# Kernel optimization log

Measured on AMD Instinct MI355X. Metric: run time of the kernel, lower is better.

## Reference

```python
import jax, jax.numpy as jnp
import numpy as np
from jax import lax

C = 16
FIRE_RATE = 0.5
STEP_SIZE = 1.0


def _fixed_kernel():
    _i = np.array([0, 1, 0], dtype=np.float32)
    I = np.outer(_i, _i)
    dx = (np.outer([1, 2, 1], [-1, 0, 1]) / 8.0).astype(np.float32)
    dy = dx.T
    lap = np.array([[0.25, 0.5, 0.25], [0.5, -3, 0.5], [0.25, 0.5, 0.25]], dtype=np.float32)
    av = np.ones((3, 3), dtype=np.float32) / 9.0
    k = np.stack([I, dx, dy, lap, av], -1)            # [3,3,5]
    k = np.tile(k, (1, 1, C))                          # [3,3,5*C], channel-major blocks of 5
    return jnp.asarray(k[:, :, None, :])               # HWIO [3,3,1,5*C]

KERNEL = _fixed_kernel()


def setup_inputs() -> dict:
    key = jax.random.key(0)
    ks = jax.random.split(key, 5)
    B, S = 4, 512
    x = jax.random.normal(ks[0], (B, S, S, C), jnp.float32)
    noise = jax.random.normal(ks[1], (B, S, S, 1), jnp.float32)
    W1 = jax.random.normal(ks[2], (5 * C, 4 * C), jnp.float32) * (1.0 / np.sqrt(5 * C))
    b1 = jnp.zeros((4 * C,), jnp.float32)
    W2 = jax.random.normal(ks[3], (4 * C, 2 * C), jnp.float32) * (1.0 / np.sqrt(4 * C))
    b2 = jnp.zeros((2 * C,), jnp.float32)
    W3 = jax.random.normal(ks[4], (2 * C, C), jnp.float32) * (1.0 / np.sqrt(2 * C))
    b3 = jnp.zeros((C,), jnp.float32)
    return {"x": x, "noise": noise, "W1": W1, "b1": b1, "W2": W2, "b2": b2, "W3": W3, "b3": b3}


def _swish(z):
    return z * jax.nn.sigmoid(z)


def reference(x, noise, W1, b1, W2, b2, W3, b3):
    # perceive: depthwise 3x3 conv with 5 fixed kernels per channel -> [B,H,W,5*C]
    y = lax.conv_general_dilated(
        x, KERNEL, window_strides=(1, 1), padding="SAME",
        dimension_numbers=("NHWC", "HWIO", "NHWC"), feature_group_count=C)
    # 3-layer 1x1 conv MLP
    h = _swish(jnp.einsum("bhwc,cd->bhwd", y, W1) + b1)
    h = _swish(jnp.einsum("bhwc,cd->bhwd", h, W2) + b2)
    dx = (jnp.einsum("bhwc,cd->bhwd", h, W3) + b3) * STEP_SIZE
    # stochastic update mask: normal noise <= fire_rate
    update_mask = (noise <= FIRE_RATE).astype(jnp.float32)  # [B,H,W,1]
    return x + dx * update_mask
```

## Files before the change

kernel.cpp:

```cpp
#include <hip/hip_runtime.h>

typedef __bf16 bf16x8 __attribute__((ext_vector_type(8)));
typedef float f32x4 __attribute__((ext_vector_type(4)));
typedef float f32x16 __attribute__((ext_vector_type(16)));
typedef short short8 __attribute__((ext_vector_type(8)));

#define S 512
#define CH 16

#define ELT(v, c) ((c)==0 ? (v).x : (c)==1 ? (v).y : (c)==2 ? (v).z : (v).w)

__device__ __forceinline__ float swishf(float z) {
    return z * __builtin_amdgcn_rcpf(1.0f + __expf(-z));
}

__global__ void prep_weights(const float* __restrict__ W1, const float* __restrict__ b1,
                             const float* __restrict__ W2, const float* __restrict__ b2,
                             const float* __restrict__ W3, const float* __restrict__ b3,
                             short* __restrict__ wsf, float* __restrict__ wsb)
{
    int idx = blockIdx.x * 256 + threadIdx.x;
    if (idx < 7680) {
        float v;
        if (idx < 5120) {
            int fi = idx >> 9, rem = idx & 511;
            int lane = rem >> 3, j = rem & 7;
            int n = fi / 5, s = fi - n * 5;
            int blk = lane >> 5, colw = lane & 31;
            int m = s * 8 + j, cc = m / 5, f = m - cc * 5;
            int row = (blk * 8 + cc) * 5 + f;
            v = W1[row * 64 + n * 32 + colw];
        } else if (idx < 7168) {
            int i2 = idx - 5120;
            int fi = i2 >> 9, rem = i2 & 511;
            int lane = rem >> 3, j = rem & 7;
            int u2 = fi >> 1, t = fi & 1;
            int k = t * 32 + (lane >> 4) * 8 + j;
            v = W2[k * 32 + u2 * 16 + (lane & 15)];
        } else {
            int i3 = idx - 7168;
            int lane = i3 >> 3, j = i3 & 7;
            int k = (lane >> 4) * 8 + j;
            v = W3[k * 16 + (lane & 15)];
        }
        __bf16 b = (__bf16)v;
        wsf[idx] = __builtin_bit_cast(short, b);
    }
    if (blockIdx.x == 0) {
        int t = threadIdx.x;
        if (t < 64) wsb[t] = b1[t];
        else if (t < 96) wsb[t] = b2[t - 64];
        else if (t < 112) wsb[t] = b3[t - 96];
    }
}

__global__ __launch_bounds__(256, 4) void nca_fused(
    const float* __restrict__ x, const float* __restrict__ noise,
    const short* __restrict__ wsf, const float* __restrict__ wsb,
    float* __restrict__ out)
{
    __shared__ short wlds[7680];
    __shared__ __bf16 h1s[4][32][72];
    __shared__ __bf16 h2s[4][16][40];

    const int tid = threadIdx.x;
    {
        const int4* src = reinterpret_cast<const int4*>(wsf);
        int4* dst = reinterpret_cast<int4*>(wlds);
        for (int i = tid; i < 960; i += 256) dst[i] = src[i];
    }
    __syncthreads();

    const int bid = blockIdx.x;
    const int st = bid & 7;
    const int rg = (bid >> 3) & 127;
    const int bb = bid >> 10;
    const int wv = tid >> 6;
    const int lane = tid & 63;
    const int col = lane & 31, hi = lane >> 5;
    const int lr = lane & 15, lg = lane >> 4;
    const int row = rg * 4 + wv;

    float b1v[2], b2v[2], b3v;
    b1v[0] = wsb[col];        b1v[1] = wsb[32 + col];
    b2v[0] = wsb[64 + lr];    b2v[1] = wsb[80 + lr];
    b3v = wsb[96 + lr];

    const bool rv0 = row > 0, rv2 = row < S - 1;
    const float* xb = x + (size_t)bb * S * S * CH;
    const short8* wf = reinterpret_cast<const short8*>(wlds);

#pragma unroll
    for (int mt = 0; mt < 2; ++mt) {
        const int px0 = st * 64 + mt * 32;
        const bool colInt = (px0 != 0) && (px0 != 480);
        const int p = col;

        short8 af[5];
#pragma unroll
        for (int qi = 0; qi < 2; ++qi) {
            const int q = hi * 2 + qi;
            float4 A[3][3];
#pragma unroll
            for (int rr = 0; rr < 3; ++rr) {
                bool rok = (rr == 0) ? rv0 : (rr == 2 ? rv2 : true);
                if (rok) {
                    const float* rp = xb + (size_t)(row - 1 + rr) * S * CH + q * 4;
                    if (colInt) {
                        const float* bp = rp + (px0 + p - 1) * CH;
                        A[rr][0] = *reinterpret_cast<const float4*>(bp);
                        A[rr][1] = *reinterpret_cast<const float4*>(bp + CH);
                        A[rr][2] = *reinterpret_cast<const float4*>(bp + 2 * CH);
                    } else {
#pragma unroll
                        for (int d = 0; d < 3; ++d) {
                            int c = px0 + p - 1 + d;
                            int cl = min(max(c, 0), S - 1);
                            float4 v = *reinterpret_cast<const float4*>(rp + cl * CH);
                            if ((unsigned)c >= (unsigned)S) v = make_float4(0.f, 0.f, 0.f, 0.f);
                            A[rr][d] = v;
                        }
                    }
                } else {
                    A[rr][0] = make_float4(0.f, 0.f, 0.f, 0.f);
                    A[rr][1] = A[rr][0]; A[rr][2] = A[rr][0];
                }
            }
#pragma unroll
            for (int cc = 0; cc < 4; ++cc) {
                float a00 = ELT(A[0][0], cc), a01 = ELT(A[0][1], cc), a02 = ELT(A[0][2], cc);
                float a10 = ELT(A[1][0], cc), a11 = ELT(A[1][1], cc), a12 = ELT(A[1][2], cc);
                float a20 = ELT(A[2][0], cc), a21 = ELT(A[2][1], cc), a22 = ELT(A[2][2], cc);
                float cw0 = a00 + 2.f * a10 + a20;
                float cw1 = a01 + 2.f * a11 + a21;
                float cw2 = a02 + 2.f * a12 + a22;
                float rw0 = a00 + 2.f * a01 + a02;
                float rw2 = a20 + 2.f * a21 + a22;
                float fI  = a11;
                float fdx = (cw2 - cw0) * 0.125f;
                float fdy = (rw2 - rw0) * 0.125f;
                float flp = 0.25f * (cw0 + 2.f * cw1 + cw2) - 4.f * a11;
                float fav = ((cw0 + cw1 + cw2) - (a10 + a11 + a12)) * (1.f / 9.f);
                const int mb = (qi * 4 + cc) * 5;
                af[(mb + 0) >> 3][(mb + 0) & 7] = __builtin_bit_cast(short, (__bf16)fI);
                af[(mb + 1) >> 3][(mb + 1) & 7] = __builtin_bit_cast(short, (__bf16)fdx);
                af[(mb + 2) >> 3][(mb + 2) & 7] = __builtin_bit_cast(short, (__bf16)fdy);
                af[(mb + 3) >> 3][(mb + 3) & 7] = __builtin_bit_cast(short, (__bf16)flp);
                af[(mb + 4) >> 3][(mb + 4) & 7] = __builtin_bit_cast(short, (__bf16)fav);
            }
        }

#pragma unroll
        for (int n = 0; n < 2; ++n) {
            f32x16 acc = {};
#pragma unroll
            for (int s = 0; s < 5; ++s) {
                bf16x8 a = __builtin_bit_cast(bf16x8, af[s]);
                bf16x8 b = __builtin_bit_cast(bf16x8, wf[(n * 5 + s) * 64 + lane]);
                acc = __builtin_amdgcn_mfma_f32_32x32x16_bf16(a, b, acc, 0, 0, 0);
            }
#pragma unroll
            for (int r = 0; r < 16; ++r) {
                int p2 = (r & 3) + 8 * (r >> 2) + 4 * hi;
                h1s[wv][p2][n * 32 + col] = (__bf16)swishf(acc[r] + b1v[n]);
            }
        }

#pragma unroll
        for (int sub = 0; sub < 2; ++sub) {
            bf16x8 a2[2];
#pragma unroll
            for (int t = 0; t < 2; ++t)
                a2[t] = *reinterpret_cast<const bf16x8*>(&h1s[wv][sub * 16 + lr][t * 32 + lg * 8]);
#pragma unroll
            for (int u2 = 0; u2 < 2; ++u2) {
                f32x4 acc2 = {};
#pragma unroll
                for (int t = 0; t < 2; ++t) {
                    bf16x8 b = __builtin_bit_cast(bf16x8, wf[640 + (u2 * 2 + t) * 64 + lane]);
                    acc2 = __builtin_amdgcn_mfma_f32_16x16x32_bf16(a2[t], b, acc2, 0, 0, 0);
                }
#pragma unroll
                for (int r = 0; r < 4; ++r)
                    h2s[wv][lg * 4 + r][u2 * 16 + lr] = (__bf16)swishf(acc2[r] + b2v[u2]);
            }
            bf16x8 a3 = *reinterpret_cast<const bf16x8*>(&h2s[wv][lr][lg * 8]);
            bf16x8 b3f = __builtin_bit_cast(bf16x8, wf[896 + lane]);
            f32x4 acc3 = {};
            acc3 = __builtin_amdgcn_mfma_f32_16x16x32_bf16(a3, b3f, acc3, 0, 0, 0);
#pragma unroll
            for (int r = 0; r < 4; ++r) {
                int pxg = px0 + sub * 16 + lg * 4 + r;
                size_t pix = (size_t)(bb * S + row) * S + pxg;
                float cx = x[pix * CH + lr];
                float msk = (noise[pix] <= 0.5f) ? 1.f : 0.f;
                out[pix * CH + lr] = cx + (acc3[r] + b3v) * msk;
            }
        }
    }
}

extern "C" void kernel_launch(void* const* d_in, const int* in_sizes, int n_in,
                              void* d_out, int out_size, void* d_ws, size_t ws_size,
                              hipStream_t stream)
{
    const float* x     = (const float*)d_in[0];
    const float* noise = (const float*)d_in[1];
    const float* W1    = (const float*)d_in[2];
    const float* b1    = (const float*)d_in[3];
    const float* W2    = (const float*)d_in[4];
    const float* b2    = (const float*)d_in[5];
    const float* W3    = (const float*)d_in[6];
    const float* b3    = (const float*)d_in[7];
    short* wsf = (short*)d_ws;
    float* wsb = (float*)((char*)d_ws + 15360);
    float* out = (float*)d_out;

    hipLaunchKernelGGL(prep_weights, dim3(30), dim3(256), 0, stream,
                       W1, b1, W2, b2, W3, b3, wsf, wsb);
    hipLaunchKernelGGL(nca_fused, dim3(4 * 128 * 8), dim3(256), 0, stream,
                       x, noise, wsf, wsb, out);
}
```

Baseline: 178.1 us.

## Transpose MLP chain so activations stay in registers between MFMA layers

Swaps the MFMA operand order so weights are the A operand and pixel features the B operand. The 32x32 accumulator layout of each layer then maps directly onto the next layer's B-fragment, which removes the h1/h2 shared-memory round trips and the layer-2/3 16x16 MFMAs. Weights are repacked to match, with W3 zero-padded to 32 columns, and output is written as float4 per lane. Each block now handles one 32-pixel tile instead of two, with twice as many blocks and launch bounds raised to 5 waves for occupancy. The cost is a padded third-layer MFMA and more register pressure.

```diff
diff --git a/kernel.cpp b/kernel.cpp
--- a/kernel.cpp
+++ b/kernel.cpp
@@ -20,28 +20,24 @@
                              short* __restrict__ wsf, float* __restrict__ wsb)
 {
     int idx = blockIdx.x * 256 + threadIdx.x;
-    if (idx < 7680) {
+    if (idx < 8192) {
+        int fi = idx >> 9, rem = idx & 511;
+        int lane = rem >> 3, j = rem & 7;
+        int col = lane & 31, hi = lane >> 5;
+        int jp = (j & 3) + 8 * (j >> 2);
         float v;
-        if (idx < 5120) {
-            int fi = idx >> 9, rem = idx & 511;
-            int lane = rem >> 3, j = rem & 7;
+        if (fi < 10) {
             int n = fi / 5, s = fi - n * 5;
-            int blk = lane >> 5, colw = lane & 31;
-            int m = s * 8 + j, cc = m / 5, f = m - cc * 5;
-            int row = (blk * 8 + cc) * 5 + f;
-            v = W1[row * 64 + n * 32 + colw];
-        } else if (idx < 7168) {
-            int i2 = idx - 5120;
-            int fi = i2 >> 9, rem = i2 & 511;
-            int lane = rem >> 3, j = rem & 7;
-            int u2 = fi >> 1, t = fi & 1;
-            int k = t * 32 + (lane >> 4) * 8 + j;
-            v = W2[k * 32 + u2 * 16 + (lane & 15)];
+            int rowW = hi * 40 + s * 8 + j;
+            v = W1[rowW * 64 + n * 32 + col];
+        } else if (fi < 14) {
+            int t = fi - 10;
+            int rowW = (t >> 1) * 32 + 4 * hi + (t & 1) * 16 + jp;
+            v = W2[rowW * 32 + col];
         } else {
-            int i3 = idx - 7168;
-            int lane = i3 >> 3, j = i3 & 7;
-            int k = (lane >> 4) * 8 + j;
-            v = W3[k * 16 + (lane & 15)];
+            int t = fi - 14;
+            int rowW = 4 * hi + t * 16 + jp;
+            v = (col < 16) ? W3[rowW * 16 + col] : 0.0f;
         }
         __bf16 b = (__bf16)v;
         wsf[idx] = __builtin_bit_cast(short, b);
@@ -54,49 +50,35 @@
     }
 }
 
-__global__ __launch_bounds__(256, 4) void nca_fused(
+__global__ __launch_bounds__(256, 5) void nca_fused(
     const float* __restrict__ x, const float* __restrict__ noise,
     const short* __restrict__ wsf, const float* __restrict__ wsb,
     float* __restrict__ out)
 {
-    __shared__ short wlds[7680];
-    __shared__ __bf16 h1s[4][32][72];
-    __shared__ __bf16 h2s[4][16][40];
-
-    const int tid = threadIdx.x;
+    __shared__ short wlds[8192];
     {
         const int4* src = reinterpret_cast<const int4*>(wsf);
         int4* dst = reinterpret_cast<int4*>(wlds);
-        for (int i = tid; i < 960; i += 256) dst[i] = src[i];
+        for (int i = threadIdx.x; i < 1024; i += 256) dst[i] = src[i];
     }
     __syncthreads();
 
+    const int tid = threadIdx.x;
     const int bid = blockIdx.x;
-    const int st = bid & 7;
-    const int rg = (bid >> 3) & 127;
-    const int bb = bid >> 10;
-    const int wv = tid >> 6;
-    const int lane = tid & 63;
+    const int st = bid & 15;
+    const int rg = (bid >> 4) & 127;
+    const int bb = bid >> 11;
+    const int wv = tid >> 6, lane = tid & 63;
     const int col = lane & 31, hi = lane >> 5;
-    const int lr = lane & 15, lg = lane >> 4;
     const int row = rg * 4 + wv;
-
-    float b1v[2], b2v[2], b3v;
-    b1v[0] = wsb[col];        b1v[1] = wsb[32 + col];
-    b2v[0] = wsb[64 + lr];    b2v[1] = wsb[80 + lr];
-    b3v = wsb[96 + lr];
-
-    const bool rv0 = row > 0, rv2 = row < S - 1;
-    const float* xb = x + (size_t)bb * S * S * CH;
-    const short8* wf = reinterpret_cast<const short8*>(wlds);
-
-#pragma unroll
-    for (int mt = 0; mt < 2; ++mt) {
-        const int px0 = st * 64 + mt * 32;
+    const int px0 = st * 32;
+
+    short8 af[5];
+    {
+        const bool rv0 = row > 0, rv2 = row < S - 1;
         const bool colInt = (px0 != 0) && (px0 != 480);
+        const float* xb = x + (size_t)bb * S * S * CH;
         const int p = col;
-
-        short8 af[5];
 #pragma unroll
         for (int qi = 0; qi < 2; ++qi) {
             const int q = hi * 2 + qi;
@@ -149,55 +131,82 @@
                 af[(mb + 4) >> 3][(mb + 4) & 7] = __builtin_bit_cast(short, (__bf16)fav);
             }
         }
-
-#pragma unroll
-        for (int n = 0; n < 2; ++n) {
-            f32x16 acc = {};
-#pragma unroll
-            for (int s = 0; s < 5; ++s) {
-                bf16x8 a = __builtin_bit_cast(bf16x8, af[s]);
-                bf16x8 b = __builtin_bit_cast(bf16x8, wf[(n * 5 + s) * 64 + lane]);
-                acc = __builtin_amdgcn_mfma_f32_32x32x16_bf16(a, b, acc, 0, 0, 0);
-            }
-#pragma unroll
-            for (int r = 0; r < 16; ++r) {
-                int p2 = (r & 3) + 8 * (r >> 2) + 4 * hi;
-                h1s[wv][p2][n * 32 + col] = (__bf16)swishf(acc[r] + b1v[n]);
-            }
-        }
-
-#pragma unroll
-        for (int sub = 0; sub < 2; ++sub) {
-            bf16x8 a2[2];
-#pragma unroll
-            for (int t = 0; t < 2; ++t)
-                a2[t] = *reinterpret_cast<const bf16x8*>(&h1s[wv][sub * 16 + lr][t * 32 + lg * 8]);
-#pragma unroll
-            for (int u2 = 0; u2 < 2; ++u2) {
-                f32x4 acc2 = {};
-#pragma unroll
-                for (int t = 0; t < 2; ++t) {
-                    bf16x8 b = __builtin_bit_cast(bf16x8, wf[640 + (u2 * 2 + t) * 64 + lane]);
-                    acc2 = __builtin_amdgcn_mfma_f32_16x16x32_bf16(a2[t], b, acc2, 0, 0, 0);
-                }
-#pragma unroll
-                for (int r = 0; r < 4; ++r)
-                    h2s[wv][lg * 4 + r][u2 * 16 + lr] = (__bf16)swishf(acc2[r] + b2v[u2]);
-            }
-            bf16x8 a3 = *reinterpret_cast<const bf16x8*>(&h2s[wv][lr][lg * 8]);
-            bf16x8 b3f = __builtin_bit_cast(bf16x8, wf[896 + lane]);
-            f32x4 acc3 = {};
-            acc3 = __builtin_amdgcn_mfma_f32_16x16x32_bf16(a3, b3f, acc3, 0, 0, 0);
-#pragma unroll
-            for (int r = 0; r < 4; ++r) {
-                int pxg = px0 + sub * 16 + lg * 4 + r;
-                size_t pix = (size_t)(bb * S + row) * S + pxg;
-                float cx = x[pix * CH + lr];
-                float msk = (noise[pix] <= 0.5f) ? 1.f : 0.f;
-                out[pix * CH + lr] = cx + (acc3[r] + b3v) * msk;
-            }
-        }
-    }
+    }
+
+    const short8* wf = reinterpret_cast<const short8*>(wlds);
+
+    f32x16 acc1[2];
+#pragma unroll
+    for (int n = 0; n < 2; ++n) {
+        f32x16 acc = {};
+#pragma unroll
+        for (int s = 0; s < 5; ++s) {
+            bf16x8 a = __builtin_bit_cast(bf16x8, wf[(n * 5 + s) * 64 + lane]);
+            bf16x8 b = __builtin_bit_cast(bf16x8, af[s]);
+            acc = __builtin_amdgcn_mfma_f32_32x32x16_bf16(a, b, acc, 0, 0, 0);
+        }
+        acc1[n] = acc;
+    }
+
+    short8 b2f[4];
+#pragma unroll
+    for (int t = 0; t < 4; ++t) {
+        int n = t >> 1;
+        float4 bq0 = *reinterpret_cast<const float4*>(wsb + n * 32 + 4 * hi + 16 * (t & 1));
+        float4 bq1 = *reinterpret_cast<const float4*>(wsb + n * 32 + 4 * hi + 16 * (t & 1) + 8);
+#pragma unroll
+        for (int j = 0; j < 8; ++j) {
+            float bias = (j < 4) ? ELT(bq0, j & 3) : ELT(bq1, j & 3);
+            float h = swishf(acc1[n][(t & 1) * 8 + j] + bias);
+            b2f[t][j] = __builtin_bit_cast(short, (__bf16)h);
+        }
+    }
+
+    f32x16 acc2 = {};
+#pragma unroll
+    for (int t = 0; t < 4; ++t) {
+        bf16x8 a = __builtin_bit_cast(bf16x8, wf[(10 + t) * 64 + lane]);
+        acc2 = __builtin_amdgcn_mfma_f32_32x32x16_bf16(a, __builtin_bit_cast(bf16x8, b2f[t]), acc2, 0, 0, 0);
+    }
+
+    short8 b3f[2];
+#pragma unroll
+    for (int t = 0; t < 2; ++t) {
+        float4 cq0 = *reinterpret_cast<const float4*>(wsb + 64 + 4 * hi + 16 * t);
+        float4 cq1 = *reinterpret_cast<const float4*>(wsb + 64 + 4 * hi + 16 * t + 8);
+#pragma unroll
+        for (int j = 0; j < 8; ++j) {
+            float bias = (j < 4) ? ELT(cq0, j & 3) : ELT(cq1, j & 3);
+            float h = swishf(acc2[t * 8 + j] + bias);
+            b3f[t][j] = __builtin_bit_cast(short, (__bf16)h);
+        }
+    }
+
+    f32x16 acc3 = {};
+#pragma unroll
+    for (int t = 0; t < 2; ++t) {
+        bf16x8 a = __builtin_bit_cast(bf16x8, wf[(14 + t) * 64 + lane]);
+        acc3 = __builtin_amdgcn_mfma_f32_32x32x16_bf16(a, __builtin_bit_cast(bf16x8, b3f[t]), acc3, 0, 0, 0);
+    }
+
+    size_t pix = ((size_t)(bb * S + row)) * S + px0 + col;
+    float msk = (noise[pix] <= 0.5f) ? 1.f : 0.f;
+    float4 bA = *reinterpret_cast<const float4*>(wsb + 96 + 4 * hi);
+    float4 bB = *reinterpret_cast<const float4*>(wsb + 96 + 8 + 4 * hi);
+    const float* xp = x + pix * CH;
+    float4 c0 = *reinterpret_cast<const float4*>(xp + 4 * hi);
+    float4 c1 = *reinterpret_cast<const float4*>(xp + 8 + 4 * hi);
+    float4 o0, o1;
+    o0.x = c0.x + (acc3[0] + bA.x) * msk;
+    o0.y = c0.y + (acc3[1] + bA.y) * msk;
+    o0.z = c0.z + (acc3[2] + bA.z) * msk;
+    o0.w = c0.w + (acc3[3] + bA.w) * msk;
+    o1.x = c1.x + (acc3[4] + bB.x) * msk;
+    o1.y = c1.y + (acc3[5] + bB.y) * msk;
+    o1.z = c1.z + (acc3[6] + bB.z) * msk;
+    o1.w = c1.w + (acc3[7] + bB.w) * msk;
+    *reinterpret_cast<float4*>(out + pix * CH + 4 * hi) = o0;
+    *reinterpret_cast<float4*>(out + pix * CH + 8 + 4 * hi) = o1;
 }
 
 extern "C" void kernel_launch(void* const* d_in, const int* in_sizes, int n_in,
@@ -213,11 +222,11 @@
     const float* W3    = (const float*)d_in[6];
     const float* b3    = (const float*)d_in[7];
     short* wsf = (short*)d_ws;
-    float* wsb = (float*)((char*)d_ws + 15360);
+    float* wsb = (float*)((char*)d_ws + 16384);
     float* out = (float*)d_out;
 
-    hipLaunchKernelGGL(prep_weights, dim3(30), dim3(256), 0, stream,
+    hipLaunchKernelGGL(prep_weights, dim3(32), dim3(256), 0, stream,
                        W1, b1, W2, b2, W3, b3, wsf, wsb);
-    hipLaunchKernelGGL(nca_fused, dim3(4 * 128 * 8), dim3(256), 0, stream,
+    hipLaunchKernelGGL(nca_fused, dim3(4 * 128 * 16), dim3(256), 0, stream,
                        x, noise, wsf, wsb, out);
 }
```

Measured after the change: 177.7 us. No clear change (-0.2%).
